# Kernel tuning notes

Measured on AMD Instinct MI355X. Metric: run time of the kernel, lower is better.

Reference implementation:

```python
import jax, jax.numpy as jnp
import numpy as np


def setup_inputs() -> dict:
    key = jax.random.key(0)
    N, nH, D, L, P = 2, 8, 32, 4, 4
    shapes = np.array([[92, 92], [46, 46], [23, 23], [12, 12]], dtype=np.int64)
    areas = shapes[:, 0] * shapes[:, 1]
    Lin = int(areas.sum())  # 11253
    Lq = Lin  # encoder self-attention
    k1, k2, k3 = jax.random.split(key, 3)
    value = jax.random.normal(k1, (N, Lin, nH, D), dtype=jnp.float32)
    sampling_locations = jax.random.uniform(k2, (N, Lq, nH, L, P, 2), dtype=jnp.float32)
    aw = jax.random.uniform(k3, (N, Lq, nH, L, P), dtype=jnp.float32)
    attention_weights = aw / aw.sum(axis=(-2, -1), keepdims=True)  # softmax-normalized over L*P
    spatial_shapes = jnp.asarray(shapes)
    starts = np.concatenate([[0], np.cumsum(areas)[:-1]])
    level_start_index = jnp.asarray(starts, dtype=jnp.int64)
    return dict(value=value, spatial_shapes=spatial_shapes,
                level_start_index=level_start_index,
                sampling_locations=sampling_locations,
                attention_weights=attention_weights)


def _gather2d(v_nh, xi, yi, Hl, Wl):
    # v_nh: [N, nH, Hl*Wl, D]; xi, yi: [N, Lq, nH, P] int32 pixel coords
    N, Lq, nH, P = xi.shape
    valid = (xi >= 0) & (xi < Wl) & (yi >= 0) & (yi < Hl)
    xc = jnp.clip(xi, 0, Wl - 1)
    yc = jnp.clip(yi, 0, Hl - 1)
    idx = (yc * Wl + xc).transpose(0, 2, 1, 3).reshape(N, nH, Lq * P)
    vals = jax.vmap(jax.vmap(lambda v, i: v[i]))(v_nh, idx)  # [N, nH, Lq*P, D]
    vals = vals.reshape(N, nH, Lq, P, -1).transpose(0, 2, 1, 3, 4)  # [N, Lq, nH, P, D]
    return vals * valid[..., None].astype(vals.dtype)


def reference(value, spatial_shapes, level_start_index, sampling_locations, attention_weights):
    # ms_deform_attn core: per-level bilinear sampling (align_corners=False,
    # zero padding) at learned locations, weighted sum over levels and points.
    shapes_np = np.asarray(spatial_shapes)
    starts_np = np.asarray(level_start_index)
    N, Lin, nH, D = value.shape
    _, Lq, _, L, P, _ = sampling_locations.shape
    out = jnp.zeros((N, Lq, nH, D), dtype=value.dtype)
    for lvl in range(L):
        Hl, Wl = int(shapes_np[lvl, 0]), int(shapes_np[lvl, 1])
        s = int(starts_np[lvl])
        v_nh = value[:, s:s + Hl * Wl].transpose(0, 2, 1, 3)  # [N, nH, Hl*Wl, D]
        loc = sampling_locations[:, :, :, lvl]  # [N, Lq, nH, P, 2]
        # grid_sample convention: normalized [0,1] -> pixel coord, align_corners=False
        x = loc[..., 0] * Wl - 0.5
        y = loc[..., 1] * Hl - 0.5
        x0f = jnp.floor(x); y0f = jnp.floor(y)
        dx = x - x0f; dy = y - y0f
        x0 = x0f.astype(jnp.int32); y0 = y0f.astype(jnp.int32)
        x1 = x0 + 1; y1 = y0 + 1
        w00 = ((1.0 - dx) * (1.0 - dy))[..., None]
        w01 = (dx * (1.0 - dy))[..., None]
        w10 = ((1.0 - dx) * dy)[..., None]
        w11 = (dx * dy)[..., None]
        samp = (w00 * _gather2d(v_nh, x0, y0, Hl, Wl)
                + w01 * _gather2d(v_nh, x1, y0, Hl, Wl)
                + w10 * _gather2d(v_nh, x0, y1, Hl, Wl)
                + w11 * _gather2d(v_nh, x1, y1, Hl, Wl))  # [N, Lq, nH, P, D]
        aw_l = attention_weights[:, :, :, lvl]  # [N, Lq, nH, P]
        out = out + (samp * aw_l[..., None]).sum(axis=3)
    return out.reshape(N, Lq, nH * D)
```

## Files before the change

### kernel.cpp

```cpp
#include <hip/hip_runtime.h>

#define NH 8
#define DD 32
#define LL 4
#define PP 4

typedef float  f32x4  __attribute__((ext_vector_type(4)));
typedef float  f32x2  __attribute__((ext_vector_type(2)));
typedef int    i32x4  __attribute__((ext_vector_type(4)));
typedef _Float16 half4v __attribute__((ext_vector_type(4)));

__global__ __launch_bounds__(256) void conv_kernel(
    const float* __restrict__ value, _Float16* __restrict__ vh,
    int Lin, int spx, int nSlabs)
{
    const int xcd  = blockIdx.x & 7;
    const int blk  = blockIdx.x >> 3;
    const int sw   = blk % spx;
    const int seg  = blk / spx;
    const int slab = xcd * spx + sw;
    if (slab >= nSlabs) return;
    const int i = seg * 256 + threadIdx.x;
    if (i >= Lin * 8) return;
    const int d4  = i & 7;
    const int pos = i >> 3;
    const int n   = slab >> 3;
    const int h   = slab & 7;

    const f32x4 v = __builtin_nontemporal_load(
        (const f32x4*)(value + (((size_t)n * Lin + pos) * NH + h) * DD + d4 * 4));
    half4v o;
    o.x = (_Float16)v.x; o.y = (_Float16)v.y; o.z = (_Float16)v.z; o.w = (_Float16)v.w;
    *(half4v*)(vh + ((size_t)slab * Lin + pos) * DD + d4 * 4) = o;
}

#define FMAMIX_LO(ACC, DW, W) \
    asm("v_fma_mix_f32 %0, %1, %2, %0 op_sel:[0,0,0] op_sel_hi:[1,0,0]" \
        : "+v"(ACC) : "v"(DW), "v"(W))
#define FMAMIX_HI(ACC, DW, W) \
    asm("v_fma_mix_f32 %0, %1, %2, %0 op_sel:[1,0,0] op_sel_hi:[1,0,0]" \
        : "+v"(ACC) : "v"(DW), "v"(W))

__global__ __attribute__((amdgpu_flat_work_group_size(256, 256)))
__attribute__((amdgpu_waves_per_eu(8)))
void msda_fwd_h(
    const _Float16* __restrict__ vh,
    const int*   __restrict__ ssh,
    const int*   __restrict__ lsi,
    const float* __restrict__ sloc,
    const float* __restrict__ aw,
    float*       __restrict__ out,
    int N, int Lq, int Lin, int spx, int nSlabs)
{
    __shared__ i32x4 ent[32 * 39];

    const int xcd   = blockIdx.x & 7;
    const int blk   = blockIdx.x >> 3;
    const int sw    = blk % spx;
    const int chunk = blk / spx;
    const int slab  = xcd * spx + sw;
    if (slab >= nSlabs) return;

    const int t  = threadIdx.x;
    const int u  = t >> 3;
    const int j  = t & 7;
    const int q  = chunk * 32 + u;
    const int qc = min(q, Lq - 1);
    const int n  = slab >> 3;
    const int h  = slab & 7;

    {
        const size_t nqh = ((size_t)n * Lq + qc) * NH + h;
        const int l = j >> 1;
        const bool is64 = (ssh[1] == 0);
        const int W = is64 ? ssh[4 * l + 2] : ssh[2 * l + 1];
        const int H = is64 ? ssh[4 * l]     : ssh[2 * l];
        const int S = is64 ? lsi[2 * l]     : lsi[l];
        const f32x4 lc = __builtin_nontemporal_load((const f32x4*)sloc + nqh * 8 + j);
        const f32x2 av = __builtin_nontemporal_load((const f32x2*)aw + nqh * 8 + j);
        const float fW = (float)W, fH = (float)H;
        const int rowb  = W * (DD * 2);
        const int sbase = S * (DD * 2);
#pragma unroll
        for (int pt = 0; pt < 2; ++pt) {
            const float x  = lc[2 * pt]     * fW - 0.5f;
            const float y  = lc[2 * pt + 1] * fH - 0.5f;
            const float wq = av[pt];
            const float x0f = floorf(x), y0f = floorf(y);
            const int x0 = (int)x0f, y0 = (int)y0f;
            const float dx = x - x0f, dy = y - y0f;
            const int x1 = x0 + 1, y1 = y0 + 1;
            const bool vx0 = (x0 >= 0) & (x0 < W), vx1 = (x1 >= 0) & (x1 < W);
            const bool vy0 = (y0 >= 0) & (y0 < H), vy1 = (y1 >= 0) & (y1 < H);
            const int cx0 = min(max(x0, 0), W - 1), cx1 = min(max(x1, 0), W - 1);
            const int cy0 = min(max(y0, 0), H - 1), cy1 = min(max(y1, 0), H - 1);
            const float wx0 = (1.f - dx) * wq * (vx0 ? 1.f : 0.f);
            const float wx1 = dx         * wq * (vx1 ? 1.f : 0.f);
            const float ty  = (1.f - dy) * (vy0 ? 1.f : 0.f);
            const float by  = dy         * (vy1 ? 1.f : 0.f);
            const int rt = cy0 * rowb + sbase;
            const int rb = cy1 * rowb + sbase;
            i32x4 e0, e1;
            e0.x = rt + cx0 * (DD * 2);  e0.y = rb + cx0 * (DD * 2);
            e0.z = __float_as_int(wx0 * ty);  e0.w = __float_as_int(wx0 * by);
            e1.x = rt + cx1 * (DD * 2);  e1.y = rb + cx1 * (DD * 2);
            e1.z = __float_as_int(wx1 * ty);  e1.w = __float_as_int(wx1 * by);
            const int base = u * 39 + 5 * j + 2 * pt;
            ent[base]     = e0;
            ent[base + 1] = e1;
        }
    }
    __syncthreads();
    if (q >= Lq) return;

    const int side = j >> 2;
    const int cg   = j & 3;
    const char* __restrict__ sb =
        (const char*)vh + (size_t)slab * Lin * (DD * 2) + cg * 16;
    const int ub = u * 39 + side;

    float acc[8];
#pragma unroll
    for (int k = 0; k < 8; ++k) acc[k] = 0.f;

#define RD(b, E) { \
    E[0] = ent[ub + 10 * (b) + 0]; \
    E[1] = ent[ub + 10 * (b) + 2]; \
    E[2] = ent[ub + 10 * (b) + 5]; \
    E[3] = ent[ub + 10 * (b) + 7]; }
#define LD(E, V) _Pragma("unroll") \
    for (int i = 0; i < 4; ++i) { \
        V[2*i]   = *(const i32x4*)(sb + (unsigned)E[i].x); \
        V[2*i+1] = *(const i32x4*)(sb + (unsigned)E[i].y); }
#define AC(E, V) _Pragma("unroll") \
    for (int i = 0; i < 4; ++i) { \
        const float wt = __int_as_float(E[i].z); \
        const float wb = __int_as_float(E[i].w); \
        _Pragma("unroll") for (int d = 0; d < 4; ++d) { \
            FMAMIX_LO(acc[2*d],   V[2*i][d],   wt); \
            FMAMIX_HI(acc[2*d+1], V[2*i][d],   wt); \
            FMAMIX_LO(acc[2*d],   V[2*i+1][d], wb); \
            FMAMIX_HI(acc[2*d+1], V[2*i+1][d], wb); } }

    i32x4 E0[4], E1[4], E2[4], E3[4];
    i32x4 V0[8], V1[8], V2[8], V3[8];
    RD(0, E0) LD(E0, V0)
    RD(1, E1) LD(E1, V1)
    AC(E0, V0)
    RD(2, E2) LD(E2, V2)
    AC(E1, V1)
    RD(3, E3) LD(E3, V3)
    AC(E2, V2)
    AC(E3, V3)

#pragma unroll
    for (int k = 0; k < 8; ++k)
        acc[k] += __shfl_xor(acc[k], 4);

    f32x4 st;
    st.x = acc[side * 4 + 0];
    st.y = acc[side * 4 + 1];
    st.z = acc[side * 4 + 2];
    st.w = acc[side * 4 + 3];
    const size_t onqh = ((size_t)n * Lq + q) * NH + h;
    __builtin_nontemporal_store(st, (f32x4*)(out + onqh * DD + cg * 8 + side * 4));
}

__global__ __launch_bounds__(256) void msda_fwd_f32(
    const float* __restrict__ value,
    const int*   __restrict__ spatial_shapes,
    const int*   __restrict__ level_start,
    const float* __restrict__ sloc,
    const float* __restrict__ aw,
    float*       __restrict__ out,
    int N, int Lq, int Lin, int total)
{
    int tid = blockIdx.x * blockDim.x + threadIdx.x;
    if (tid >= total) return;
    const int c  = tid & 7;
    const int h  = (tid >> 3) & 7;
    const int nq = tid >> 6;
    const int n  = nq / Lq;
    const bool is64 = (spatial_shapes[1] == 0);
    int Hs[LL], Ws[LL], Ss[LL];
#pragma unroll
    for (int l = 0; l < LL; ++l) {
        if (is64) { Hs[l] = spatial_shapes[4*l]; Ws[l] = spatial_shapes[4*l+2]; Ss[l] = level_start[2*l]; }
        else      { Hs[l] = spatial_shapes[2*l]; Ws[l] = spatial_shapes[2*l+1]; Ss[l] = level_start[l]; }
    }
    const size_t nqh = (size_t)nq * NH + h;
    const float* loc_p = sloc + nqh * (LL * PP * 2);
    const float* aw_p  = aw   + nqh * (LL * PP);
    float4 acc = make_float4(0.f, 0.f, 0.f, 0.f);
#pragma unroll
    for (int l = 0; l < LL; ++l) {
        const int H = Hs[l], W = Ws[l];
        const float* vb = value + (((size_t)n * Lin + Ss[l]) * NH + h) * DD + c * 4;
#pragma unroll
        for (int p = 0; p < PP; ++p) {
            const int jj = l * PP + p;
            const float x = loc_p[2*jj] * (float)W - 0.5f;
            const float y = loc_p[2*jj+1] * (float)H - 0.5f;
            const float w = aw_p[jj];
            const float x0f = floorf(x), y0f = floorf(y);
            const int x0 = (int)x0f, y0 = (int)y0f, x1 = x0+1, y1 = y0+1;
            const float dx = x - x0f, dy = y - y0f;
            const bool vx0 = x0>=0 && x0<W, vx1 = x1>=0 && x1<W;
            const bool vy0 = y0>=0 && y0<H, vy1 = y1>=0 && y1<H;
            const int cx0 = min(max(x0,0),W-1), cx1 = min(max(x1,0),W-1);
            const int cy0 = min(max(y0,0),H-1), cy1 = min(max(y1,0),H-1);
            const float w00 = (1.f-dx)*(1.f-dy)*w*((vx0&&vy0)?1.f:0.f);
            const float w01 = dx*(1.f-dy)*w*((vx1&&vy0)?1.f:0.f);
            const float w10 = (1.f-dx)*dy*w*((vx0&&vy1)?1.f:0.f);
            const float w11 = dx*dy*w*((vx1&&vy1)?1.f:0.f);
            const float4 v00 = *(const float4*)(vb + (size_t)(cy0*W+cx0)*(NH*DD));
            const float4 v01 = *(const float4*)(vb + (size_t)(cy0*W+cx1)*(NH*DD));
            const float4 v10 = *(const float4*)(vb + (size_t)(cy1*W+cx0)*(NH*DD));
            const float4 v11 = *(const float4*)(vb + (size_t)(cy1*W+cx1)*(NH*DD));
            acc.x += w00*v00.x + w01*v01.x + w10*v10.x + w11*v11.x;
            acc.y += w00*v00.y + w01*v01.y + w10*v10.y + w11*v11.y;
            acc.z += w00*v00.z + w01*v01.z + w10*v10.z + w11*v11.z;
            acc.w += w00*v00.w + w01*v01.w + w10*v10.w + w11*v11.w;
        }
    }
    *(float4*)(out + nqh * DD + c * 4) = acc;
}

extern "C" void kernel_launch(void* const* d_in, const int* in_sizes, int n_in,
                              void* d_out, int out_size, void* d_ws, size_t ws_size,
                              hipStream_t stream)
{
    const float* value = (const float*)d_in[0];
    const int*   ss    = (const int*)  d_in[1];
    const int*   lsi   = (const int*)  d_in[2];
    const float* sloc  = (const float*)d_in[3];
    const float* aw    = (const float*)d_in[4];
    float* out = (float*)d_out;

    const int N = 2;
    const int Lq  = in_sizes[4] / (N * NH * LL * PP);
    const int Lin = in_sizes[0] / (N * NH * DD);

    const size_t need = (size_t)N * NH * Lin * DD * sizeof(_Float16);
    if (ws_size >= need) {
        _Float16* vh = (_Float16*)d_ws;
        const int nSlabs = N * NH;
        const int spx    = (nSlabs + 7) / 8;
        const int segs   = (Lin * 8 + 255) / 256;
        conv_kernel<<<8 * spx * segs, 256, 0, stream>>>(value, vh, Lin, spx, nSlabs);

        const int chunks = (Lq + 31) / 32;
        const int grid   = 8 * spx * chunks;
        msda_fwd_h<<<grid, 256, 0, stream>>>(vh, ss, lsi, sloc, aw, out,
                                             N, Lq, Lin, spx, nSlabs);
    } else {
        const int total = N * Lq * NH * 8;
        msda_fwd_f32<<<(total + 255) / 256, 256, 0, stream>>>(value, ss, lsi, sloc, aw, out,
                                                              N, Lq, Lin, total);
    }
}
```

Measured before the change: 144.1 us.

## Process two query chunks per block with prefetched inputs and scheduling barriers

Each block now handles two 32-query chunks instead of one, halving the grid. The sampling-location and attention-weight loads for both chunks are issued up front, so the second chunk's inputs are in flight while the first chunk is computed. Scheduling barriers pin the order of LDS entry reads, gathers and FMAs, and the value buffers are reused between stages to cut register use. The occupancy hint drops from 8 to 4 waves per EU, trading latency hiding across waves for more per-thread work, and the block-wide sync is removed because each 8-lane group only reads LDS entries written within its own wave.

```diff
diff --git a/kernel.cpp b/kernel.cpp
--- a/kernel.cpp
+++ b/kernel.cpp
@@ -41,8 +41,10 @@
     asm("v_fma_mix_f32 %0, %1, %2, %0 op_sel:[1,0,0] op_sel_hi:[1,0,0]" \
         : "+v"(ACC) : "v"(DW), "v"(W))
 
+#define SB() __builtin_amdgcn_sched_barrier(0)
+
 __global__ __attribute__((amdgpu_flat_work_group_size(256, 256)))
-__attribute__((amdgpu_waves_per_eu(8)))
+__attribute__((amdgpu_waves_per_eu(4)))
 void msda_fwd_h(
     const _Float16* __restrict__ vh,
     const int*   __restrict__ ssh,
@@ -50,78 +52,79 @@
     const float* __restrict__ sloc,
     const float* __restrict__ aw,
     float*       __restrict__ out,
-    int N, int Lq, int Lin, int spx, int nSlabs)
+    int N, int Lq, int Lin, int spx, int half, int nSlabs)
 {
     __shared__ i32x4 ent[32 * 39];
 
-    const int xcd   = blockIdx.x & 7;
-    const int blk   = blockIdx.x >> 3;
-    const int sw    = blk % spx;
-    const int chunk = blk / spx;
-    const int slab  = xcd * spx + sw;
+    const int xcd  = blockIdx.x & 7;
+    const int blk  = blockIdx.x >> 3;
+    const int sw   = blk / half;
+    const int c2   = blk % half;
+    const int slab = xcd * spx + sw;
     if (slab >= nSlabs) return;
 
     const int t  = threadIdx.x;
     const int u  = t >> 3;
     const int j  = t & 7;
-    const int q  = chunk * 32 + u;
-    const int qc = min(q, Lq - 1);
     const int n  = slab >> 3;
     const int h  = slab & 7;
 
-    {
-        const size_t nqh = ((size_t)n * Lq + qc) * NH + h;
-        const int l = j >> 1;
-        const bool is64 = (ssh[1] == 0);
-        const int W = is64 ? ssh[4 * l + 2] : ssh[2 * l + 1];
-        const int H = is64 ? ssh[4 * l]     : ssh[2 * l];
-        const int S = is64 ? lsi[2 * l]     : lsi[l];
-        const f32x4 lc = __builtin_nontemporal_load((const f32x4*)sloc + nqh * 8 + j);
-        const f32x2 av = __builtin_nontemporal_load((const f32x2*)aw + nqh * 8 + j);
-        const float fW = (float)W, fH = (float)H;
-        const int rowb  = W * (DD * 2);
-        const int sbase = S * (DD * 2);
-#pragma unroll
-        for (int pt = 0; pt < 2; ++pt) {
-            const float x  = lc[2 * pt]     * fW - 0.5f;
-            const float y  = lc[2 * pt + 1] * fH - 0.5f;
-            const float wq = av[pt];
-            const float x0f = floorf(x), y0f = floorf(y);
-            const int x0 = (int)x0f, y0 = (int)y0f;
-            const float dx = x - x0f, dy = y - y0f;
-            const int x1 = x0 + 1, y1 = y0 + 1;
-            const bool vx0 = (x0 >= 0) & (x0 < W), vx1 = (x1 >= 0) & (x1 < W);
-            const bool vy0 = (y0 >= 0) & (y0 < H), vy1 = (y1 >= 0) & (y1 < H);
-            const int cx0 = min(max(x0, 0), W - 1), cx1 = min(max(x1, 0), W - 1);
-            const int cy0 = min(max(y0, 0), H - 1), cy1 = min(max(y1, 0), H - 1);
-            const float wx0 = (1.f - dx) * wq * (vx0 ? 1.f : 0.f);
-            const float wx1 = dx         * wq * (vx1 ? 1.f : 0.f);
-            const float ty  = (1.f - dy) * (vy0 ? 1.f : 0.f);
-            const float by  = dy         * (vy1 ? 1.f : 0.f);
-            const int rt = cy0 * rowb + sbase;
-            const int rb = cy1 * rowb + sbase;
-            i32x4 e0, e1;
-            e0.x = rt + cx0 * (DD * 2);  e0.y = rb + cx0 * (DD * 2);
-            e0.z = __float_as_int(wx0 * ty);  e0.w = __float_as_int(wx0 * by);
-            e1.x = rt + cx1 * (DD * 2);  e1.y = rb + cx1 * (DD * 2);
-            e1.z = __float_as_int(wx1 * ty);  e1.w = __float_as_int(wx1 * by);
-            const int base = u * 39 + 5 * j + 2 * pt;
-            ent[base]     = e0;
-            ent[base + 1] = e1;
-        }
-    }
-    __syncthreads();
-    if (q >= Lq) return;
+    const int q0 = (2 * c2) * 32 + u;
+    const int q1 = (2 * c2 + 1) * 32 + u;
+    const int q0c = min(q0, Lq - 1);
+    const int q1c = min(q1, Lq - 1);
+
+    const size_t nqh0 = ((size_t)n * Lq + q0c) * NH + h;
+    const size_t nqh1 = ((size_t)n * Lq + q1c) * NH + h;
+    const f32x4 lc0 = __builtin_nontemporal_load((const f32x4*)sloc + nqh0 * 8 + j);
+    const f32x2 av0 = __builtin_nontemporal_load((const f32x2*)aw + nqh0 * 8 + j);
+    const f32x4 lc1 = __builtin_nontemporal_load((const f32x4*)sloc + nqh1 * 8 + j);
+    const f32x2 av1 = __builtin_nontemporal_load((const f32x2*)aw + nqh1 * 8 + j);
+
+    const int l = j >> 1;
+    const bool is64 = (ssh[1] == 0);
+    const int W = is64 ? ssh[4 * l + 2] : ssh[2 * l + 1];
+    const int H = is64 ? ssh[4 * l]     : ssh[2 * l];
+    const int S = is64 ? lsi[2 * l]     : lsi[l];
+    const float fW = (float)W, fH = (float)H;
+    const int rowb  = W * (DD * 2);
+    const int sbase = S * (DD * 2);
+
+#define PHASE1(LC, AV) { \
+        _Pragma("unroll") \
+        for (int pt = 0; pt < 2; ++pt) { \
+            const float x  = LC[2 * pt]     * fW - 0.5f; \
+            const float y  = LC[2 * pt + 1] * fH - 0.5f; \
+            const float wq = AV[pt]; \
+            const float x0f = floorf(x), y0f = floorf(y); \
+            const int x0 = (int)x0f, y0 = (int)y0f; \
+            const float dx = x - x0f, dy = y - y0f; \
+            const int x1 = x0 + 1, y1 = y0 + 1; \
+            const bool vx0 = (x0 >= 0) & (x0 < W), vx1 = (x1 >= 0) & (x1 < W); \
+            const bool vy0 = (y0 >= 0) & (y0 < H), vy1 = (y1 >= 0) & (y1 < H); \
+            const int cx0 = min(max(x0, 0), W - 1), cx1 = min(max(x1, 0), W - 1); \
+            const int cy0 = min(max(y0, 0), H - 1), cy1 = min(max(y1, 0), H - 1); \
+            const float wx0 = (1.f - dx) * wq * (vx0 ? 1.f : 0.f); \
+            const float wx1 = dx         * wq * (vx1 ? 1.f : 0.f); \
+            const float ty  = (1.f - dy) * (vy0 ? 1.f : 0.f); \
+            const float by  = dy         * (vy1 ? 1.f : 0.f); \
+            const int rt = cy0 * rowb + sbase; \
+            const int rb = cy1 * rowb + sbase; \
+            i32x4 e0, e1; \
+            e0.x = rt + cx0 * (DD * 2);  e0.y = rb + cx0 * (DD * 2); \
+            e0.z = __float_as_int(wx0 * ty);  e0.w = __float_as_int(wx0 * by); \
+            e1.x = rt + cx1 * (DD * 2);  e1.y = rb + cx1 * (DD * 2); \
+            e1.z = __float_as_int(wx1 * ty);  e1.w = __float_as_int(wx1 * by); \
+            const int base = u * 39 + 5 * j + 2 * pt; \
+            ent[base]     = e0; \
+            ent[base + 1] = e1; \
+        } }
 
     const int side = j >> 2;
     const int cg   = j & 3;
     const char* __restrict__ sb =
         (const char*)vh + (size_t)slab * Lin * (DD * 2) + cg * 16;
     const int ub = u * 39 + side;
-
-    float acc[8];
-#pragma unroll
-    for (int k = 0; k < 8; ++k) acc[k] = 0.f;
 
 #define RD(b, E) { \
     E[0] = ent[ub + 10 * (b) + 0]; \
@@ -142,28 +145,53 @@
             FMAMIX_LO(acc[2*d],   V[2*i+1][d], wb); \
             FMAMIX_HI(acc[2*d+1], V[2*i+1][d], wb); } }
 
-    i32x4 E0[4], E1[4], E2[4], E3[4];
-    i32x4 V0[8], V1[8], V2[8], V3[8];
-    RD(0, E0) LD(E0, V0)
-    RD(1, E1) LD(E1, V1)
-    AC(E0, V0)
-    RD(2, E2) LD(E2, V2)
-    AC(E1, V1)
-    RD(3, E3) LD(E3, V3)
-    AC(E2, V2)
-    AC(E3, V3)
-
-#pragma unroll
-    for (int k = 0; k < 8; ++k)
-        acc[k] += __shfl_xor(acc[k], 4);
-
-    f32x4 st;
-    st.x = acc[side * 4 + 0];
-    st.y = acc[side * 4 + 1];
-    st.z = acc[side * 4 + 2];
-    st.w = acc[side * 4 + 3];
-    const size_t onqh = ((size_t)n * Lq + q) * NH + h;
-    __builtin_nontemporal_store(st, (f32x4*)(out + onqh * DD + cg * 8 + side * 4));
+#define PHASE2() { \
+    i32x4 E0[4], E1[4], E2[4], E3[4]; \
+    i32x4 V0[8], V1[8]; \
+    RD(0, E0) RD(1, E1) \
+    SB(); \
+    LD(E0, V0) LD(E1, V1) \
+    SB(); \
+    AC(E0, V0) \
+    RD(2, E2) \
+    SB(); \
+    LD(E2, V0) \
+    SB(); \
+    AC(E1, V1) \
+    RD(3, E3) \
+    SB(); \
+    LD(E3, V1) \
+    SB(); \
+    AC(E2, V0) \
+    AC(E3, V1) }
+
+#define MERGE_STORE(Q) { \
+    _Pragma("unroll") \
+    for (int k = 0; k < 8; ++k) \
+        acc[k] += __shfl_xor(acc[k], 4); \
+    if ((Q) < Lq) { \
+        f32x4 st; \
+        st.x = acc[side * 4 + 0]; \
+        st.y = acc[side * 4 + 1]; \
+        st.z = acc[side * 4 + 2]; \
+        st.w = acc[side * 4 + 3]; \
+        const size_t onqh = ((size_t)n * Lq + (Q)) * NH + h; \
+        __builtin_nontemporal_store(st, (f32x4*)(out + onqh * DD + cg * 8 + side * 4)); \
+    } }
+
+    float acc[8];
+
+    PHASE1(lc0, av0)
+#pragma unroll
+    for (int k = 0; k < 8; ++k) acc[k] = 0.f;
+    PHASE2()
+    MERGE_STORE(q0)
+
+    PHASE1(lc1, av1)
+#pragma unroll
+    for (int k = 0; k < 8; ++k) acc[k] = 0.f;
+    PHASE2()
+    MERGE_STORE(q1)
 }
 
 __global__ __launch_bounds__(256) void msda_fwd_f32(
@@ -250,9 +278,10 @@
         conv_kernel<<<8 * spx * segs, 256, 0, stream>>>(value, vh, Lin, spx, nSlabs);
 
         const int chunks = (Lq + 31) / 32;
-        const int grid   = 8 * spx * chunks;
+        const int half   = (chunks + 1) / 2;
+        const int grid   = 8 * spx * half;
         msda_fwd_h<<<grid, 256, 0, stream>>>(vh, ss, lsi, sloc, aw, out,
-                                             N, Lq, Lin, spx, nSlabs);
+                                             N, Lq, Lin, spx, half, nSlabs);
     } else {
         const int total = N * Lq * NH * 8;
         msda_fwd_f32<<<(total + 255) / 256, 256, 0, stream>>>(value, ss, lsi, sloc, aw, out,
```

Measured after the change: 140.4 us. 2.5% less time.
